# Kernel tuning notes

Hardware: AMD Instinct MI355X
Metric: run time of the kernel (lower is better)

## Reference

```python
import jax, jax.numpy as jnp
import numpy as np

N, B, NPG = 65536, 512, 128      # total nodes, graphs, nodes per graph
E, EPG = 524288, 1024            # total edges, edges per graph
D, R, L = 64, 16, 3              # emb_dim, num relations, encoder layers
PHI = 0.1
EPS_VAR = 1e-5


def _mean_std(x):
    # torch.var is unbiased (ddof=1); keep last-dim stats per row
    m = jnp.mean(x, axis=-1, keepdims=True)
    s = jnp.sqrt(jnp.var(x, axis=-1, ddof=1, keepdims=True) + EPS_VAR)
    return m, s


def _rgcn_encode(feat, Wrel, Wself, b, src, dst, etype, edge_w):
    """L-layer relational GCN. Returns (last_h [N,D], repr [N,L,D])."""
    h = feat
    reps = []
    for l in range(L):
        hr = jnp.einsum('nd,rdk->nrk', h, Wrel[l])        # [N,R,D]
        msg = hr[src, etype]                               # [E,D] per-edge typed transform
        msg = msg * edge_w[:, None]
        agg = jax.ops.segment_sum(msg, dst, num_segments=N)
        deg = jax.ops.segment_sum(edge_w, dst, num_segments=N)
        h = jax.nn.relu(h @ Wself[l] + agg / jnp.clip(deg, 1.0)[:, None] + b[l])
        reps.append(h)
    return h, jnp.stack(reps, axis=1)


def _pool(rep, node_gid):
    # mean_nodes over 'repr': graphs have fixed NPG nodes
    s = jax.ops.segment_sum(rep.reshape(N, L * D), node_gid, num_segments=B)
    return (s / NPG).reshape(B, L, D)


def full_forward(feat, rel_feat, rel_proj_W, rel_proj_b, rgcn_Wrel, rgcn_Wself,
                 rgcn_b, enc_W_mean, enc_W_std, dec_Wh, dec_bh, dec_Wt, dec_bt,
                 dec_Wr, dec_br, fc_W, fc_b, eps,
                 src, dst, etype, aug_src, aug_dst, aug_etype, node_gid, rel_labels):
    ones_e = jnp.ones((E,), feat.dtype)
    # relation encoder + projection
    emb_rel = jax.nn.relu(rel_feat @ rel_proj_W + rel_proj_b)          # [R,D]
    # encode original and augmented graphs
    x, rep_g = _rgcn_encode(feat, rgcn_Wrel, rgcn_Wself, rgcn_b, src, dst, etype, ones_e)
    g_out = _pool(rep_g, node_gid)
    aug_x, rep_aug = _rgcn_encode(feat, rgcn_Wrel, rgcn_Wself, rgcn_b, aug_src, aug_dst, aug_etype, ones_e)
    aug_g_out = _pool(rep_aug, node_gid)
    # AdaIn style transfer (args.interp == False)
    mc, sc = _mean_std(x)
    ms, ss = _mean_std(aug_x)
    style_applied = ss * ((x - mc) / sc) + ms
    # VAE reparameterization
    z_mean = style_applied @ enc_W_mean
    z_std = style_applied @ enc_W_std
    z = z_mean + jnp.sqrt(jnp.exp(z_std)) * eps
    # decoder: edge-level DistMult scoring -> edge mask
    head_e = jax.nn.relu(z[src] @ dec_Wh + dec_bh)                     # [E,D]
    tail_e = jax.nn.relu(z[dst] @ dec_Wt + dec_bt)
    rel_e = jax.nn.relu(emb_rel[etype] @ dec_Wr + dec_br)
    logit = jnp.sum(head_e * rel_e * tail_e, axis=-1)                  # [E]
    mask = (logit >= 0.5).astype(feat.dtype)
    # root edge (edge_ids(0,1)) = first edge of each graph, forced kept
    mask = mask.at[jnp.arange(B) * EPG].set(1.0)
    # re-encode reconstructed (masked) graph with original features
    x_recon, rep_recon = _rgcn_encode(feat, rgcn_Wrel, rgcn_Wself, rgcn_b, src, dst, etype, mask)
    recon_g_out = _pool(rep_recon, node_gid)
    # head node (id==1) = node 0 of each graph; tail (id==2) = node 1
    head_ids = jnp.arange(B) * NPG
    tail_ids = head_ids + 1
    g_rep = jnp.concatenate([
        recon_g_out.reshape(B, L * D),
        rep_recon[head_ids].reshape(B, L * D),
        rep_recon[tail_ids].reshape(B, L * D),
        emb_rel[rel_labels],
    ], axis=1)                                                          # [B, 3*L*D + D]
    output = g_rep @ fc_W + fc_b                                        # [B,1]
    # reconstruction + style losses, summed over layers
    mse_per_layer = jnp.mean((rep_recon - rep_g) ** 2, axis=(0, 2))     # [L]
    mr, sr = _mean_std(rep_recon.transpose(1, 0, 2))                    # [L,N,1]
    mg, sg = _mean_std(rep_g.transpose(1, 0, 2))
    style_per_layer = jnp.mean((mr - mg) ** 2, axis=(1, 2)) + jnp.mean((sr - sg) ** 2, axis=(1, 2))
    loss = jnp.sum(mse_per_layer) + PHI * jnp.sum(style_per_layer)
    return output, g_out, aug_g_out, loss


def setup_inputs() -> dict:
    key = jax.random.key(0)
    ks = jax.random.split(key, 28)
    egid = jnp.arange(E, dtype=jnp.int32) // EPG
    node_gid = jnp.arange(N, dtype=jnp.int32) // NPG
    mk_edges = lambda k1, k2: (egid * NPG + jax.random.randint(k1, (E,), 0, NPG, jnp.int32),
                               egid * NPG + jax.random.randint(k2, (E,), 0, NPG, jnp.int32))
    src, dst = mk_edges(ks[0], ks[1])
    aug_src, aug_dst = mk_edges(ks[2], ks[3])
    g = lambda i, shape, s=0.05: (jax.random.normal(ks[i], shape, jnp.float32) * s)
    return {
        'feat': g(4, (N, D), 1.0),
        'rel_feat': g(5, (R, 64), 1.0),
        'rel_proj_W': g(6, (64, D)),
        'rel_proj_b': jnp.zeros((D,), jnp.float32),
        'rgcn_Wrel': g(7, (L, R, D, D)),
        'rgcn_Wself': g(8, (L, D, D)),
        'rgcn_b': jnp.zeros((L, D), jnp.float32),
        'enc_W_mean': g(9, (D, D)),
        'enc_W_std': g(10, (D, D)),
        'dec_Wh': g(11, (D, D), 0.1),
        'dec_bh': jnp.zeros((D,), jnp.float32),
        'dec_Wt': g(12, (D, D), 0.1),
        'dec_bt': jnp.zeros((D,), jnp.float32),
        'dec_Wr': g(13, (D, D), 0.1),
        'dec_br': jnp.zeros((D,), jnp.float32),
        'fc_W': g(14, (3 * L * D + D, 1)),
        'fc_b': jnp.zeros((1,), jnp.float32),
        'eps': g(15, (N, D), 1.0),
        'src': src, 'dst': dst,
        'etype': jax.random.randint(ks[16], (E,), 0, R, jnp.int32),
        'aug_src': aug_src, 'aug_dst': aug_dst,
        'aug_etype': jax.random.randint(ks[17], (E,), 0, R, jnp.int32),
        'node_gid': node_gid,
        'rel_labels': jax.random.randint(ks[18], (B,), 0, R, jnp.int32),
    }


def reference(feat, rel_feat, rel_proj_W, rel_proj_b, rgcn_Wrel, rgcn_Wself,
              rgcn_b, enc_W_mean, enc_W_std, dec_Wh, dec_bh, dec_Wt, dec_bt,
              dec_Wr, dec_br, fc_W, fc_b, eps,
              src, dst, etype, aug_src, aug_dst, aug_etype, node_gid, rel_labels):
    return full_forward(feat, rel_feat, rel_proj_W, rel_proj_b, rgcn_Wrel, rgcn_Wself,
                        rgcn_b, enc_W_mean, enc_W_std, dec_Wh, dec_bh, dec_Wt, dec_bt,
                        dec_Wr, dec_br, fc_W, fc_b, eps,
                        src, dst, etype, aug_src, aug_dst, aug_etype, node_gid, rel_labels)
```

## Files before the change

kernel.cpp:

```cpp
#include <hip/hip_runtime.h>
#include <hip/hip_bf16.h>

typedef __attribute__((ext_vector_type(8))) short bf16x8;
typedef __attribute__((ext_vector_type(4))) float f32x4;

#define NPG  128
#define EPG  1024
#define BG   512
#define NT   512
#define NW   8
#define PHI  0.1f
#define EPSV 1e-5f
#define SB   72
#define SF   65

#define OUT_G    512
#define OUT_AUG  98816
#define OUT_LOSS 197120
#define WS_EMB   0
#define WS_RELE  1024
#define WS_LOSSP 2048
#define WS_REPG  4096

__device__ __forceinline__ unsigned short f2bf(float x) {
  __hip_bfloat16 h = __float2bfloat16(x);
  return *reinterpret_cast<unsigned short*>(&h);
}
__device__ __forceinline__ float bf2f(unsigned short u) {
  __hip_bfloat16 h = *reinterpret_cast<__hip_bfloat16*>(&u);
  return __bfloat162float(h);
}
__device__ __forceinline__ void split_write(unsigned short* hh, unsigned short* hl,
                                            int idx, float x) {
  unsigned short hi = f2bf(x);
  hh[idx] = hi;
  hl[idx] = f2bf(x - bf2f(hi));
}

#define LOAD_BF(Wp, ctn, ks, bhv, blv)                                         \
  {                                                                            \
    bf16x8 h_, l_;                                                             \
    _Pragma("unroll") for (int j_ = 0; j_ < 8; j_++) {                         \
      float w_ = (Wp)[((ks) * 32 + kg * 8 + j_) * 64 + (ctn) * 16 + n];        \
      unsigned short hi_ = f2bf(w_);                                           \
      h_[j_] = (short)hi_;                                                     \
      l_[j_] = (short)f2bf(w_ - bf2f(hi_));                                    \
    }                                                                          \
    bhv = h_;                                                                  \
    blv = l_;                                                                  \
  }

__device__ __forceinline__ f32x4 mfma3(bf16x8 a0h, bf16x8 a1h, bf16x8 a0l, bf16x8 a1l,
                                       bf16x8 b0h, bf16x8 b1h, bf16x8 b0l, bf16x8 b1l,
                                       f32x4 acc) {
  acc = __builtin_amdgcn_mfma_f32_16x16x32_bf16(a0h, b0h, acc, 0, 0, 0);
  acc = __builtin_amdgcn_mfma_f32_16x16x32_bf16(a1h, b1h, acc, 0, 0, 0);
  acc = __builtin_amdgcn_mfma_f32_16x16x32_bf16(a0h, b0l, acc, 0, 0, 0);
  acc = __builtin_amdgcn_mfma_f32_16x16x32_bf16(a1h, b1l, acc, 0, 0, 0);
  acc = __builtin_amdgcn_mfma_f32_16x16x32_bf16(a0l, b0h, acc, 0, 0, 0);
  acc = __builtin_amdgcn_mfma_f32_16x16x32_bf16(a1l, b1h, acc, 0, 0, 0);
  return acc;
}

__global__ __launch_bounds__(256) void k_prologue(
    const float* __restrict__ rel_feat, const float* __restrict__ rpW,
    const float* __restrict__ rpb, const float* __restrict__ dWr,
    const float* __restrict__ dbr, float* __restrict__ ws) {
  __shared__ float emb[1024];
  int tid = threadIdx.x;
  for (int idx = tid; idx < 1024; idx += 256) {
    int r = idx >> 6, j = idx & 63;
    float s = rpb[j];
    for (int k = 0; k < 64; k++) s = fmaf(rel_feat[r * 64 + k], rpW[k * 64 + j], s);
    s = fmaxf(s, 0.f);
    emb[idx] = s;
    ws[WS_EMB + idx] = s;
  }
  __syncthreads();
  for (int idx = tid; idx < 1024; idx += 256) {
    int r = idx >> 6, j = idx & 63;
    float s = dbr[j];
    for (int k = 0; k < 64; k++) s = fmaf(emb[r * 64 + k], dWr[k * 64 + j], s);
    ws[WS_RELE + idx] = fmaxf(s, 0.f);
  }
}

__global__ __launch_bounds__(512) void k_fin(const float* __restrict__ ws,
                                             float* __restrict__ out) {
  __shared__ float red[8];
  int tid = threadIdx.x;
  float x = ws[WS_LOSSP + tid];
#pragma unroll
  for (int o = 32; o > 0; o >>= 1) x += __shfl_down(x, o);
  if ((tid & 63) == 0) red[tid >> 6] = x;
  __syncthreads();
  if (tid == 0) {
    float s = 0.f;
#pragma unroll
    for (int w = 0; w < 8; w++) s += red[w];
    out[OUT_LOSS] = s;
  }
}

__device__ void build_elist(unsigned* elist, int* cnt, int* offs, float* dinv,
                            const unsigned* maskbits, int useMask,
                            const int* __restrict__ et_a, const int* __restrict__ src_a,
                            const int* __restrict__ dst_a, int ge, int gn, int tid) {
  if (tid < 16) cnt[tid] = 0;
  if (tid >= 128 && tid < 256) dinv[tid - 128] = 0.f;
  __syncthreads();
  for (int i = tid; i < EPG; i += NT) {
    int keep = useMask ? (int)((maskbits[i >> 5] >> (i & 31)) & 1u) : 1;
    if (keep) {
      atomicAdd(&cnt[et_a[ge + i]], 1);
      atomicAdd(&dinv[dst_a[ge + i] - gn], 1.f);
    }
  }
  __syncthreads();
  if (tid == 0) {
    int o = 0;
#pragma unroll
    for (int r = 0; r < 16; r++) { offs[r] = o; o += (cnt[r] + 15) & ~15; }
    offs[16] = o;
  }
  if (tid >= 128 && tid < 256) {
    int v = tid - 128;
    dinv[v] = 1.0f / fmaxf(dinv[v], 1.0f);
  }
  __syncthreads();
  int total = offs[16];
  for (int s = tid; s < total; s += NT) elist[s] = 128u;
  if (tid < 16) cnt[tid] = offs[tid];
  __syncthreads();
  for (int i = tid; i < EPG; i += NT) {
    int keep = useMask ? (int)((maskbits[i >> 5] >> (i & 31)) & 1u) : 1;
    if (keep) {
      int r = et_a[ge + i];
      int pos = atomicAdd(&cnt[r], 1);
      elist[pos] = ((unsigned)(src_a[ge + i] - gn) << 8) | (unsigned)(dst_a[ge + i] - gn);
    }
  }
  __syncthreads();
}

__device__ void rgcn_layer_mfma(unsigned short* hh, unsigned short* hl, float* hf32,
                                const float* dinv, const unsigned* elist,
                                const int* offs,
                                const float* __restrict__ Wl,
                                const float* __restrict__ Wsl,
                                const float* __restrict__ bl, int tid) {
  int lane = tid & 63, wave = tid >> 6;
  int n = lane & 15, kg = lane >> 4;
  for (int i = tid; i < NPG * SF; i += NT) hf32[i] = 0.f;
  __syncthreads();
  for (int r = wave; r < 16; r += NW) {
    int base = offs[r], end = offs[r + 1];
    if (base >= end) continue;
    const float* __restrict__ W = Wl + (r << 12);
#pragma unroll 1
    for (int ch = 0; ch < 2; ch++) {
      bf16x8 bh00, bh01, bl00, bl01, bh10, bh11, bl10, bl11;
      LOAD_BF(W, ch * 2 + 0, 0, bh00, bl00);
      LOAD_BF(W, ch * 2 + 0, 1, bh01, bl01);
      LOAD_BF(W, ch * 2 + 1, 0, bh10, bl10);
      LOAD_BF(W, ch * 2 + 1, 1, bh11, bl11);
      for (int tb = base; tb < end; tb += 16) {
        unsigned e = elist[tb + n];
        int srow = (int)(e >> 8);
        const unsigned short* rh = hh + srow * SB;
        const unsigned short* rl = hl + srow * SB;
        bf16x8 a0h = *(const bf16x8*)(rh + kg * 8);
        bf16x8 a1h = *(const bf16x8*)(rh + 32 + kg * 8);
        bf16x8 a0l = *(const bf16x8*)(rl + kg * 8);
        bf16x8 a1l = *(const bf16x8*)(rl + 32 + kg * 8);
        f32x4 acc0 = {0.f, 0.f, 0.f, 0.f}, acc1 = {0.f, 0.f, 0.f, 0.f};
        acc0 = mfma3(a0h, a1h, a0l, a1l, bh00, bh01, bl00, bl01, acc0);
        acc1 = mfma3(a0h, a1h, a0l, a1l, bh10, bh11, bl10, bl11, acc1);
#pragma unroll
        for (int i = 0; i < 4; i++) {
          int dst = (int)(elist[tb + kg * 4 + i] & 255u);
          if (dst < 128) {
            float* hp = hf32 + dst * SF + ch * 32 + n;
            atomicAdd(hp, acc0[i]);
            atomicAdd(hp + 16, acc1[i]);
          }
        }
      }
    }
  }
  __syncthreads();
  {
    const unsigned short* rh = hh + (wave * 16 + n) * SB;
    const unsigned short* rl = hl + (wave * 16 + n) * SB;
    bf16x8 a0h = *(const bf16x8*)(rh + kg * 8);
    bf16x8 a1h = *(const bf16x8*)(rh + 32 + kg * 8);
    bf16x8 a0l = *(const bf16x8*)(rl + kg * 8);
    bf16x8 a1l = *(const bf16x8*)(rl + 32 + kg * 8);
#pragma unroll 1
    for (int ch = 0; ch < 2; ch++) {
      bf16x8 bh00, bh01, bl00, bl01, bh10, bh11, bl10, bl11;
      LOAD_BF(Wsl, ch * 2 + 0, 0, bh00, bl00);
      LOAD_BF(Wsl, ch * 2 + 0, 1, bh01, bl01);
      LOAD_BF(Wsl, ch * 2 + 1, 0, bh10, bl10);
      LOAD_BF(Wsl, ch * 2 + 1, 1, bh11, bl11);
      f32x4 acc0 = {0.f, 0.f, 0.f, 0.f}, acc1 = {0.f, 0.f, 0.f, 0.f};
      acc0 = mfma3(a0h, a1h, a0l, a1l, bh00, bh01, bl00, bl01, acc0);
      acc1 = mfma3(a0h, a1h, a0l, a1l, bh10, bh11, bl10, bl11, acc1);
#pragma unroll
      for (int i = 0; i < 4; i++) {
        int node = wave * 16 + kg * 4 + i;
        float di = dinv[node];
#pragma unroll
        for (int c = 0; c < 2; c++) {
          int col = (ch * 2 + c) * 16 + n;
          float a = c ? acc1[i] : acc0[i];
          float v = a + hf32[node * SF + col] * di + bl[col];
          v = fmaxf(v, 0.f);
          hf32[node * SF + col] = v;
          split_write(hh, hl, node * SB + col, v);
        }
      }
    }
  }
  __syncthreads();
}

__device__ void dense_mfma(const unsigned short* ah, const unsigned short* al,
                           float* hf32, unsigned short* oh, unsigned short* ol,
                           const float* __restrict__ W, const float* __restrict__ bias,
                           int mode, const float* __restrict__ epsbuf, int gn, int tid) {
  int lane = tid & 63, wave = tid >> 6;
  int n = lane & 15, kg = lane >> 4;
  const unsigned short* rh = ah + (wave * 16 + n) * SB;
  const unsigned short* rl = al + (wave * 16 + n) * SB;
  bf16x8 a0h = *(const bf16x8*)(rh + kg * 8);
  bf16x8 a1h = *(const bf16x8*)(rh + 32 + kg * 8);
  bf16x8 a0l = *(const bf16x8*)(rl + kg * 8);
  bf16x8 a1l = *(const bf16x8*)(rl + 32 + kg * 8);
#pragma unroll 1
  for (int ch = 0; ch < 2; ch++) {
    bf16x8 bh00, bh01, bl00, bl01, bh10, bh11, bl10, bl11;
    LOAD_BF(W, ch * 2 + 0, 0, bh00, bl00);
    LOAD_BF(W, ch * 2 + 0, 1, bh01, bl01);
    LOAD_BF(W, ch * 2 + 1, 0, bh10, bl10);
    LOAD_BF(W, ch * 2 + 1, 1, bh11, bl11);
    f32x4 acc0 = {0.f, 0.f, 0.f, 0.f}, acc1 = {0.f, 0.f, 0.f, 0.f};
    acc0 = mfma3(a0h, a1h, a0l, a1l, bh00, bh01, bl00, bl01, acc0);
    acc1 = mfma3(a0h, a1h, a0l, a1l, bh10, bh11, bl10, bl11, acc1);
#pragma unroll
    for (int i = 0; i < 4; i++) {
      int node = wave * 16 + kg * 4 + i;
#pragma unroll
      for (int c = 0; c < 2; c++) {
        int col = (ch * 2 + c) * 16 + n;
        float a = c ? acc1[i] : acc0[i];
        if (mode == 0) {
          hf32[node * SF + col] = a;
        } else if (mode == 2) {
          hf32[node * SF + col] += sqrtf(expf(a)) * epsbuf[(gn + node) * 64 + col];
        } else {
          a = fmaxf(a + bias[col], 0.f);
          if (oh) split_write(oh, ol, node * SB + col, a);
          else hf32[node * SF + col] = a;
        }
      }
    }
  }
  __syncthreads();
}

__device__ void pool_sf(const float* hf32, float* red, float* dst, int tid) {
  int j = tid & 63, grp = tid >> 6;
  float s = 0.f;
  for (int v = grp * 16; v < grp * 16 + 16; v++) s += hf32[v * SF + j];
  red[tid] = s;
  __syncthreads();
  if (tid < 64) {
    float t = 0.f;
#pragma unroll
    for (int w = 0; w < NW; w++) t += red[w * 64 + tid];
    dst[tid] = t * (1.f / 128.f);
  }
  __syncthreads();
}

__global__ __launch_bounds__(NT, 2) void k_mega(
    const float* __restrict__ feat, const float* __restrict__ Wrel,
    const float* __restrict__ Wself, const float* __restrict__ bvec,
    const float* __restrict__ encWm, const float* __restrict__ encWs,
    const float* __restrict__ decWh, const float* __restrict__ dbh,
    const float* __restrict__ decWt, const float* __restrict__ dbt,
    const float* __restrict__ fcW, const float* __restrict__ fcb,
    const float* __restrict__ epsbuf,
    const int* __restrict__ srcA, const int* __restrict__ dstA, const int* __restrict__ etA,
    const int* __restrict__ asrcA, const int* __restrict__ adstA, const int* __restrict__ aetA,
    const int* __restrict__ rel_labels, float* __restrict__ ws, float* __restrict__ out) {
  __shared__ __align__(16) unsigned short hh[NPG * SB];
  __shared__ __align__(16) unsigned short hl[NPG * SB];
  __shared__ __align__(16) float hf32[NPG * SF];
  __shared__ __align__(16) unsigned elist[1280];
  __shared__ float dinv[NPG];
  __shared__ float red[NT];
  __shared__ float ht[384];
  __shared__ float rgout[192];
  __shared__ unsigned maskbits[EPG / 32];
  __shared__ int cnt[16], offs[17];

  int g = blockIdx.x, tid = threadIdx.x;
  int gn = g * NPG, ge = g * EPG;
  float* repg = ws + WS_REPG;
  float loss_acc = 0.f;

  build_elist(elist, cnt, offs, dinv, maskbits, 0, etA, srcA, dstA, ge, gn, tid);
  for (int i = tid; i < 8192; i += NT)
    split_write(hh, hl, (i >> 6) * SB + (i & 63), feat[gn * 64 + i]);
  __syncthreads();
  for (int l = 0; l < 3; l++) {
    rgcn_layer_mfma(hh, hl, hf32, dinv, elist, offs, Wrel + l * 65536,
                    Wself + l * 4096, bvec + l * 64, tid);
    for (int i = tid; i < 8192; i += NT)
      repg[(gn + (i >> 6)) * 192 + l * 64 + (i & 63)] = hf32[(i >> 6) * SF + (i & 63)];
    pool_sf(hf32, red, out + OUT_G + g * 192 + l * 64, tid);
  }
  build_elist(elist, cnt, offs, dinv, maskbits, 0, aetA, asrcA, adstA, ge, gn, tid);
  for (int i = tid; i < 8192; i += NT)
    split_write(hh, hl, (i >> 6) * SB + (i & 63), feat[gn * 64 + i]);
  __syncthreads();
  for (int l = 0; l < 3; l++) {
    rgcn_layer_mfma(hh, hl, hf32, dinv, elist, offs, Wrel + l * 65536,
                    Wself + l * 4096, bvec + l * 64, tid);
    pool_sf(hf32, red, out + OUT_AUG + g * 192 + l * 64, tid);
  }
  if (tid < NPG) {
    int v = tid;
    float t1 = 0.f, t2 = 0.f;
    for (int jj = 0; jj < 64; jj++) {
      int j = (v + jj) & 63;
      float y = hf32[v * SF + j];
      t1 += y; t2 += y * y;
    }
    float ms = t1 * (1.f / 64.f);
    red[v] = ms;
    red[NPG + v] = sqrtf((t2 - 64.f * ms * ms) * (1.f / 63.f) + EPSV);
  }
  __syncthreads();
  for (int i = tid; i < 8192; i += NT)
    hf32[(i >> 6) * SF + (i & 63)] = repg[(gn + (i >> 6)) * 192 + 128 + (i & 63)];
  __syncthreads();
  if (tid < NPG) {
    int v = tid;
    float s1 = 0.f, s2 = 0.f;
    for (int jj = 0; jj < 64; jj++) {
      int j = (v + jj) & 63;
      float x = hf32[v * SF + j];
      s1 += x; s2 += x * x;
    }
    float mc = s1 * (1.f / 64.f);
    float sc = sqrtf((s2 - 64.f * mc * mc) * (1.f / 63.f) + EPSV);
    float sca = red[NPG + v] / sc, ms = red[v];
    for (int jj = 0; jj < 64; jj++) {
      int j = (v + jj) & 63;
      hf32[v * SF + j] = (hf32[v * SF + j] - mc) * sca + ms;
    }
  }
  __syncthreads();
  for (int i = tid; i < 8192; i += NT)
    split_write(hh, hl, (i >> 6) * SB + (i & 63), hf32[(i >> 6) * SF + (i & 63)]);
  __syncthreads();
  dense_mfma(hh, hl, hf32, nullptr, nullptr, encWm, nullptr, 0, nullptr, gn, tid);
  dense_mfma(hh, hl, hf32, nullptr, nullptr, encWs, nullptr, 2, epsbuf, gn, tid);
  for (int i = tid; i < 8192; i += NT)
    split_write(hh, hl, (i >> 6) * SB + (i & 63), hf32[(i >> 6) * SF + (i & 63)]);
  __syncthreads();
  dense_mfma(hh, hl, hf32, nullptr, nullptr, decWt, dbt, 1, nullptr, gn, tid);
  dense_mfma(hh, hl, hf32, hh, hl, decWh, dbh, 1, nullptr, gn, tid);
  float* relEl = (float*)elist;
  for (int i = tid; i < 1024; i += NT) relEl[i] = ws[WS_RELE + i];
  for (int i = tid; i < EPG / 32; i += NT) maskbits[i] = 0u;
  __syncthreads();
  for (int i = tid; i < EPG; i += NT) {
    int s = srcA[ge + i] - gn, t = dstA[ge + i] - gn, r = etA[ge + i];
    int rot = (s + t) & 63;
    float lg = 0.f;
    for (int jj = 0; jj < 64; jj++) {
      int j = (rot + jj) & 63;
      float zhv = bf2f(hh[s * SB + j]) + bf2f(hl[s * SB + j]);
      lg = fmaf(zhv * hf32[t * SF + j], relEl[(r << 6) + j], lg);
    }
    if (lg >= 0.5f) atomicOr(&maskbits[i >> 5], 1u << (i & 31));
  }
  __syncthreads();
  if (tid == 0) maskbits[0] |= 1u;
  __syncthreads();
  build_elist(elist, cnt, offs, dinv, maskbits, 1, etA, srcA, dstA, ge, gn, tid);
  for (int i = tid; i < 8192; i += NT)
    split_write(hh, hl, (i >> 6) * SB + (i & 63), feat[gn * 64 + i]);
  __syncthreads();
  const float c1 = 1.0f / (65536.0f * 64.0f);
  const float c2 = PHI / 65536.0f;
  for (int l = 0; l < 3; l++) {
    rgcn_layer_mfma(hh, hl, hf32, dinv, elist, offs, Wrel + l * 65536,
                    Wself + l * 4096, bvec + l * 64, tid);
    pool_sf(hf32, red, rgout + l * 64, tid);
    if (tid < 128)
      ht[(l * 2 + (tid >> 6)) * 64 + (tid & 63)] = hf32[(tid >> 6) * SF + (tid & 63)];
    {
      int v = tid >> 2, q = tid & 3;
      const float* gp = repg + (gn + v) * 192 + l * 64 + q * 16;
      const float* hp = hf32 + v * SF + q * 16;
      float mse = 0.f, a1 = 0.f, a2 = 0.f, b1 = 0.f, b2 = 0.f;
#pragma unroll
      for (int u = 0; u < 16; u++) {
        float rc = hp[u];
        float gg = gp[u];
        float d = rc - gg;
        mse += d * d; a1 += rc; a2 += rc * rc; b1 += gg; b2 += gg * gg;
      }
#pragma unroll
      for (int m = 1; m < 4; m <<= 1) {
        mse += __shfl_xor(mse, m); a1 += __shfl_xor(a1, m); a2 += __shfl_xor(a2, m);
        b1 += __shfl_xor(b1, m); b2 += __shfl_xor(b2, m);
      }
      if (q == 0) {
        float mr = a1 * (1.f / 64.f), mg = b1 * (1.f / 64.f);
        float sr = sqrtf((a2 - 64.f * mr * mr) * (1.f / 63.f) + EPSV);
        float sg = sqrtf((b2 - 64.f * mg * mg) * (1.f / 63.f) + EPSV);
        float style = (mr - mg) * (mr - mg) + (sr - sg) * (sr - sg);
        red[v] = mse * c1 + style * c2;
      }
    }
    __syncthreads();
    if (tid < 64) {
      float x = red[tid] + red[tid + 64];
#pragma unroll
      for (int o = 32; o > 0; o >>= 1) x += __shfl_down(x, o);
      if (tid == 0) loss_acc += x;
    }
    __syncthreads();
  }
  if (tid == 0) ws[WS_LOSSP + g] = loss_acc;
  if (tid < 64) {
    int rl = rel_labels[g];
    const float* emb = ws + WS_EMB + rl * 64;
    float s = 0.f;
    for (int p = 0; p < 10; p++) {
      int i = p * 64 + tid;
      float gr;
      if (i < 192) gr = rgout[i];
      else if (i < 384) { int i2 = i - 192; gr = ht[((i2 >> 6) * 2 + 0) * 64 + (i2 & 63)]; }
      else if (i < 576) { int i2 = i - 384; gr = ht[((i2 >> 6) * 2 + 1) * 64 + (i2 & 63)]; }
      else gr = emb[i - 576];
      s = fmaf(gr, fcW[i], s);
    }
#pragma unroll
    for (int o = 32; o > 0; o >>= 1) s += __shfl_down(s, o);
    if (tid == 0) out[g] = s + fcb[0];
  }
}

extern "C" void kernel_launch(void* const* d_in, const int* in_sizes, int n_in,
                              void* d_out, int out_size, void* d_ws, size_t ws_size,
                              hipStream_t stream) {
  const float* feat     = (const float*)d_in[0];
  const float* rel_feat = (const float*)d_in[1];
  const float* rpW      = (const float*)d_in[2];
  const float* rpb      = (const float*)d_in[3];
  const float* Wrel     = (const float*)d_in[4];
  const float* Wself    = (const float*)d_in[5];
  const float* bvec     = (const float*)d_in[6];
  const float* encWm    = (const float*)d_in[7];
  const float* encWs    = (const float*)d_in[8];
  const float* decWh    = (const float*)d_in[9];
  const float* dbh      = (const float*)d_in[10];
  const float* decWt    = (const float*)d_in[11];
  const float* dbt      = (const float*)d_in[12];
  const float* decWr    = (const float*)d_in[13];
  const float* dbr      = (const float*)d_in[14];
  const float* fcW      = (const float*)d_in[15];
  const float* fcb      = (const float*)d_in[16];
  const float* epsb     = (const float*)d_in[17];
  const int* srcA  = (const int*)d_in[18];
  const int* dstA  = (const int*)d_in[19];
  const int* etA   = (const int*)d_in[20];
  const int* asrcA = (const int*)d_in[21];
  const int* adstA = (const int*)d_in[22];
  const int* aetA  = (const int*)d_in[23];
  const int* rel_labels = (const int*)d_in[25];
  float* out = (float*)d_out;
  float* ws  = (float*)d_ws;

  k_prologue<<<1, 256, 0, stream>>>(rel_feat, rpW, rpb, decWr, dbr, ws);
  k_mega<<<BG, NT, 0, stream>>>(feat, Wrel, Wself, bvec, encWm, encWs, decWh, dbh,
                                decWt, dbt, fcW, fcb, epsb, srcA, dstA, etA,
                                asrcA, adstA, aetA, rel_labels, ws, out);
  k_fin<<<1, 512, 0, stream>>>(ws, out);
}
```

Measured before the change: 1.584 ms.

## Aggregate source features per relation before transform, then one dense MFMA per relation

Reorders the RGCN message passing so raw source features are scatter-added per relation into a shared fp32 buffer, then multiplied by that relation's weight with MFMA, instead of running MFMA per edge tile and atomically scattering the outputs. The relation loop now runs sequentially across the whole block, with a buffer clear and barriers per relation. The fp32 node-state buffer is dropped in favour of reconstructing values from the hi/lo bf16 split, and the VAE dense stages are fused into two paired phases. This cuts MFMA work and edge-list padding, but adds 16 serialized clear/scatter/barrier rounds per layer and extra atomics on raw features. Aggregating before the transform also changes rounding, since sums are re-split into bf16 hi/lo before the multiply.

```diff
diff --git a/kernel.cpp b/kernel.cpp
--- a/kernel.cpp
+++ b/kernel.cpp
@@ -3,6 +3,7 @@
 
 typedef __attribute__((ext_vector_type(8))) short bf16x8;
 typedef __attribute__((ext_vector_type(4))) float f32x4;
+typedef __attribute__((ext_vector_type(4))) short short4v;
 
 #define NPG  128
 #define EPG  1024
@@ -12,7 +13,7 @@
 #define PHI  0.1f
 #define EPSV 1e-5f
 #define SB   72
-#define SF   65
+#define SS   68
 
 #define OUT_G    512
 #define OUT_AUG  98816
@@ -35,6 +36,22 @@
   unsigned short hi = f2bf(x);
   hh[idx] = hi;
   hl[idx] = f2bf(x - bf2f(hi));
+}
+__device__ __forceinline__ float recon(const unsigned short* hh,
+                                       const unsigned short* hl, int idx) {
+  return bf2f(hh[idx]) + bf2f(hl[idx]);
+}
+
+__device__ __forceinline__ void split_frag(const float* p, bf16x8& ah, bf16x8& al) {
+  float4 v0 = *(const float4*)(p);
+  float4 v1 = *(const float4*)(p + 4);
+  float vv[8] = {v0.x, v0.y, v0.z, v0.w, v1.x, v1.y, v1.z, v1.w};
+#pragma unroll
+  for (int j = 0; j < 8; j++) {
+    unsigned short hi = f2bf(vv[j]);
+    ah[j] = (short)hi;
+    al[j] = (short)f2bf(vv[j] - bf2f(hi));
+  }
 }
 
 #define LOAD_BF(Wp, ctn, ks, bhv, blv)                                         \
@@ -120,7 +137,7 @@
   if (tid == 0) {
     int o = 0;
 #pragma unroll
-    for (int r = 0; r < 16; r++) { offs[r] = o; o += (cnt[r] + 15) & ~15; }
+    for (int r = 0; r < 16; r++) { offs[r] = o; o += cnt[r]; }
     offs[16] = o;
   }
   if (tid >= 128 && tid < 256) {
@@ -128,8 +145,6 @@
     dinv[v] = 1.0f / fmaxf(dinv[v], 1.0f);
   }
   __syncthreads();
-  int total = offs[16];
-  for (int s = tid; s < total; s += NT) elist[s] = 128u;
   if (tid < 16) cnt[tid] = offs[tid];
   __syncthreads();
   for (int i = tid; i < EPG; i += NT) {
@@ -143,52 +158,52 @@
   __syncthreads();
 }
 
-__device__ void rgcn_layer_mfma(unsigned short* hh, unsigned short* hl, float* hf32,
-                                const float* dinv, const unsigned* elist,
-                                const int* offs,
-                                const float* __restrict__ Wl,
-                                const float* __restrict__ Wsl,
-                                const float* __restrict__ bl, int tid) {
+__device__ void rgcn_layer_dense(unsigned short* hh, unsigned short* hl, float* S,
+                                 const float* dinv, const unsigned* elist,
+                                 const int* offs,
+                                 const float* __restrict__ Wl,
+                                 const float* __restrict__ Wsl,
+                                 const float* __restrict__ bl, int tid) {
   int lane = tid & 63, wave = tid >> 6;
   int n = lane & 15, kg = lane >> 4;
-  for (int i = tid; i < NPG * SF; i += NT) hf32[i] = 0.f;
-  __syncthreads();
-  for (int r = wave; r < 16; r += NW) {
+  f32x4 agg[4];
+#pragma unroll
+  for (int ct = 0; ct < 4; ct++) agg[ct] = (f32x4){0.f, 0.f, 0.f, 0.f};
+
+  for (int r = 0; r < 16; r++) {
     int base = offs[r], end = offs[r + 1];
-    if (base >= end) continue;
-    const float* __restrict__ W = Wl + (r << 12);
+    if (base == end) continue;
+    for (int i = tid; i < NPG * SS; i += NT) S[i] = 0.f;
+    __syncthreads();
+    int tasks = (end - base) << 4;
+    for (int t = tid; t < tasks; t += NT) {
+      int e = base + (t >> 4), c4 = (t & 15) << 2;
+      unsigned ed = elist[e];
+      int src = (int)(ed >> 8), dst = (int)(ed & 255u);
+      short4v vh = *(const short4v*)(hh + src * SB + c4);
+      short4v vl = *(const short4v*)(hl + src * SB + c4);
+      float* ps = S + dst * SS + c4;
+#pragma unroll
+      for (int k2 = 0; k2 < 4; k2++)
+        atomicAdd(ps + k2, bf2f((unsigned short)vh[k2]) + bf2f((unsigned short)vl[k2]));
+    }
+    __syncthreads();
+    {
+      const float* sr = S + (wave * 16 + n) * SS;
+      bf16x8 a0h, a0l, a1h, a1l;
+      split_frag(sr + kg * 8, a0h, a0l);
+      split_frag(sr + 32 + kg * 8, a1h, a1l);
+      const float* __restrict__ W = Wl + (r << 12);
 #pragma unroll 1
-    for (int ch = 0; ch < 2; ch++) {
-      bf16x8 bh00, bh01, bl00, bl01, bh10, bh11, bl10, bl11;
-      LOAD_BF(W, ch * 2 + 0, 0, bh00, bl00);
-      LOAD_BF(W, ch * 2 + 0, 1, bh01, bl01);
-      LOAD_BF(W, ch * 2 + 1, 0, bh10, bl10);
-      LOAD_BF(W, ch * 2 + 1, 1, bh11, bl11);
-      for (int tb = base; tb < end; tb += 16) {
-        unsigned e = elist[tb + n];
-        int srow = (int)(e >> 8);
-        const unsigned short* rh = hh + srow * SB;
-        const unsigned short* rl = hl + srow * SB;
-        bf16x8 a0h = *(const bf16x8*)(rh + kg * 8);
-        bf16x8 a1h = *(const bf16x8*)(rh + 32 + kg * 8);
-        bf16x8 a0l = *(const bf16x8*)(rl + kg * 8);
-        bf16x8 a1l = *(const bf16x8*)(rl + 32 + kg * 8);
-        f32x4 acc0 = {0.f, 0.f, 0.f, 0.f}, acc1 = {0.f, 0.f, 0.f, 0.f};
-        acc0 = mfma3(a0h, a1h, a0l, a1l, bh00, bh01, bl00, bl01, acc0);
-        acc1 = mfma3(a0h, a1h, a0l, a1l, bh10, bh11, bl10, bl11, acc1);
-#pragma unroll
-        for (int i = 0; i < 4; i++) {
-          int dst = (int)(elist[tb + kg * 4 + i] & 255u);
-          if (dst < 128) {
-            float* hp = hf32 + dst * SF + ch * 32 + n;
-            atomicAdd(hp, acc0[i]);
-            atomicAdd(hp + 16, acc1[i]);
-          }
-        }
+      for (int ct = 0; ct < 4; ct++) {
+        bf16x8 bh0, bl0, bh1, bl1;
+        LOAD_BF(W, ct, 0, bh0, bl0);
+        LOAD_BF(W, ct, 1, bh1, bl1);
+        agg[ct] = mfma3(a0h, a1h, a0l, a1l, bh0, bh1, bl0, bl1, agg[ct]);
       }
     }
-  }
-  __syncthreads();
+    __syncthreads();
+  }
   {
     const unsigned short* rh = hh + (wave * 16 + n) * SB;
     const unsigned short* rl = hl + (wave * 16 + n) * SB;
@@ -196,83 +211,106 @@
     bf16x8 a1h = *(const bf16x8*)(rh + 32 + kg * 8);
     bf16x8 a0l = *(const bf16x8*)(rl + kg * 8);
     bf16x8 a1l = *(const bf16x8*)(rl + 32 + kg * 8);
+    f32x4 sf[4];
 #pragma unroll 1
-    for (int ch = 0; ch < 2; ch++) {
-      bf16x8 bh00, bh01, bl00, bl01, bh10, bh11, bl10, bl11;
-      LOAD_BF(Wsl, ch * 2 + 0, 0, bh00, bl00);
-      LOAD_BF(Wsl, ch * 2 + 0, 1, bh01, bl01);
-      LOAD_BF(Wsl, ch * 2 + 1, 0, bh10, bl10);
-      LOAD_BF(Wsl, ch * 2 + 1, 1, bh11, bl11);
-      f32x4 acc0 = {0.f, 0.f, 0.f, 0.f}, acc1 = {0.f, 0.f, 0.f, 0.f};
-      acc0 = mfma3(a0h, a1h, a0l, a1l, bh00, bh01, bl00, bl01, acc0);
-      acc1 = mfma3(a0h, a1h, a0l, a1l, bh10, bh11, bl10, bl11, acc1);
-#pragma unroll
-      for (int i = 0; i < 4; i++) {
-        int node = wave * 16 + kg * 4 + i;
-        float di = dinv[node];
-#pragma unroll
-        for (int c = 0; c < 2; c++) {
-          int col = (ch * 2 + c) * 16 + n;
-          float a = c ? acc1[i] : acc0[i];
-          float v = a + hf32[node * SF + col] * di + bl[col];
-          v = fmaxf(v, 0.f);
-          hf32[node * SF + col] = v;
-          split_write(hh, hl, node * SB + col, v);
-        }
+    for (int ct = 0; ct < 4; ct++) {
+      bf16x8 bh0, bl0, bh1, bl1;
+      LOAD_BF(Wsl, ct, 0, bh0, bl0);
+      LOAD_BF(Wsl, ct, 1, bh1, bl1);
+      sf[ct] = mfma3(a0h, a1h, a0l, a1l, bh0, bh1, bl0, bl1,
+                     (f32x4){0.f, 0.f, 0.f, 0.f});
+    }
+#pragma unroll
+    for (int i = 0; i < 4; i++) {
+      int node = wave * 16 + kg * 4 + i;
+      float di = dinv[node];
+#pragma unroll
+      for (int ct = 0; ct < 4; ct++) {
+        int col = ct * 16 + n;
+        float v = sf[ct][i] + agg[ct][i] * di + bl[col];
+        split_write(hh, hl, node * SB + col, fmaxf(v, 0.f));
       }
     }
   }
   __syncthreads();
 }
 
-__device__ void dense_mfma(const unsigned short* ah, const unsigned short* al,
-                           float* hf32, unsigned short* oh, unsigned short* ol,
-                           const float* __restrict__ W, const float* __restrict__ bias,
-                           int mode, const float* __restrict__ epsbuf, int gn, int tid) {
+__device__ void vae_phaseA(unsigned short* hh, unsigned short* hl,
+                           const float* __restrict__ Wm, const float* __restrict__ Wsd,
+                           const float* __restrict__ epsbuf, int gn, int tid) {
   int lane = tid & 63, wave = tid >> 6;
   int n = lane & 15, kg = lane >> 4;
-  const unsigned short* rh = ah + (wave * 16 + n) * SB;
-  const unsigned short* rl = al + (wave * 16 + n) * SB;
+  const unsigned short* rh = hh + (wave * 16 + n) * SB;
+  const unsigned short* rl = hl + (wave * 16 + n) * SB;
   bf16x8 a0h = *(const bf16x8*)(rh + kg * 8);
   bf16x8 a1h = *(const bf16x8*)(rh + 32 + kg * 8);
   bf16x8 a0l = *(const bf16x8*)(rl + kg * 8);
   bf16x8 a1l = *(const bf16x8*)(rl + 32 + kg * 8);
+  f32x4 am[4], as[4];
 #pragma unroll 1
-  for (int ch = 0; ch < 2; ch++) {
-    bf16x8 bh00, bh01, bl00, bl01, bh10, bh11, bl10, bl11;
-    LOAD_BF(W, ch * 2 + 0, 0, bh00, bl00);
-    LOAD_BF(W, ch * 2 + 0, 1, bh01, bl01);
-    LOAD_BF(W, ch * 2 + 1, 0, bh10, bl10);
-    LOAD_BF(W, ch * 2 + 1, 1, bh11, bl11);
-    f32x4 acc0 = {0.f, 0.f, 0.f, 0.f}, acc1 = {0.f, 0.f, 0.f, 0.f};
-    acc0 = mfma3(a0h, a1h, a0l, a1l, bh00, bh01, bl00, bl01, acc0);
-    acc1 = mfma3(a0h, a1h, a0l, a1l, bh10, bh11, bl10, bl11, acc1);
-#pragma unroll
-    for (int i = 0; i < 4; i++) {
-      int node = wave * 16 + kg * 4 + i;
-#pragma unroll
-      for (int c = 0; c < 2; c++) {
-        int col = (ch * 2 + c) * 16 + n;
-        float a = c ? acc1[i] : acc0[i];
-        if (mode == 0) {
-          hf32[node * SF + col] = a;
-        } else if (mode == 2) {
-          hf32[node * SF + col] += sqrtf(expf(a)) * epsbuf[(gn + node) * 64 + col];
-        } else {
-          a = fmaxf(a + bias[col], 0.f);
-          if (oh) split_write(oh, ol, node * SB + col, a);
-          else hf32[node * SF + col] = a;
-        }
-      }
-    }
-  }
-  __syncthreads();
-}
-
-__device__ void pool_sf(const float* hf32, float* red, float* dst, int tid) {
+  for (int ct = 0; ct < 4; ct++) {
+    bf16x8 bh0, bl0, bh1, bl1;
+    LOAD_BF(Wm, ct, 0, bh0, bl0);
+    LOAD_BF(Wm, ct, 1, bh1, bl1);
+    am[ct] = mfma3(a0h, a1h, a0l, a1l, bh0, bh1, bl0, bl1, (f32x4){0.f, 0.f, 0.f, 0.f});
+    LOAD_BF(Wsd, ct, 0, bh0, bl0);
+    LOAD_BF(Wsd, ct, 1, bh1, bl1);
+    as[ct] = mfma3(a0h, a1h, a0l, a1l, bh0, bh1, bl0, bl1, (f32x4){0.f, 0.f, 0.f, 0.f});
+  }
+#pragma unroll
+  for (int i = 0; i < 4; i++) {
+    int node = wave * 16 + kg * 4 + i;
+#pragma unroll
+    for (int ct = 0; ct < 4; ct++) {
+      int col = ct * 16 + n;
+      float z = am[ct][i] + sqrtf(expf(as[ct][i])) * epsbuf[(gn + node) * 64 + col];
+      split_write(hh, hl, node * SB + col, z);
+    }
+  }
+  __syncthreads();
+}
+
+__device__ void vae_phaseB(unsigned short* hh, unsigned short* hl, float* S,
+                           const float* __restrict__ Wt, const float* __restrict__ bt,
+                           const float* __restrict__ Wh, const float* __restrict__ bh_,
+                           int tid) {
+  int lane = tid & 63, wave = tid >> 6;
+  int n = lane & 15, kg = lane >> 4;
+  const unsigned short* rh = hh + (wave * 16 + n) * SB;
+  const unsigned short* rl = hl + (wave * 16 + n) * SB;
+  bf16x8 a0h = *(const bf16x8*)(rh + kg * 8);
+  bf16x8 a1h = *(const bf16x8*)(rh + 32 + kg * 8);
+  bf16x8 a0l = *(const bf16x8*)(rl + kg * 8);
+  bf16x8 a1l = *(const bf16x8*)(rl + 32 + kg * 8);
+  f32x4 at[4], ah[4];
+#pragma unroll 1
+  for (int ct = 0; ct < 4; ct++) {
+    bf16x8 bh0, bl0, bh1, bl1;
+    LOAD_BF(Wt, ct, 0, bh0, bl0);
+    LOAD_BF(Wt, ct, 1, bh1, bl1);
+    at[ct] = mfma3(a0h, a1h, a0l, a1l, bh0, bh1, bl0, bl1, (f32x4){0.f, 0.f, 0.f, 0.f});
+    LOAD_BF(Wh, ct, 0, bh0, bl0);
+    LOAD_BF(Wh, ct, 1, bh1, bl1);
+    ah[ct] = mfma3(a0h, a1h, a0l, a1l, bh0, bh1, bl0, bl1, (f32x4){0.f, 0.f, 0.f, 0.f});
+  }
+#pragma unroll
+  for (int i = 0; i < 4; i++) {
+    int node = wave * 16 + kg * 4 + i;
+#pragma unroll
+    for (int ct = 0; ct < 4; ct++) {
+      int col = ct * 16 + n;
+      S[node * SS + col] = fmaxf(at[ct][i] + bt[col], 0.f);
+      split_write(hh, hl, node * SB + col, fmaxf(ah[ct][i] + bh_[col], 0.f));
+    }
+  }
+  __syncthreads();
+}
+
+__device__ void pool_hl(const unsigned short* hh, const unsigned short* hl,
+                        float* red, float* dst, int tid) {
   int j = tid & 63, grp = tid >> 6;
   float s = 0.f;
-  for (int v = grp * 16; v < grp * 16 + 16; v++) s += hf32[v * SF + j];
+  for (int v = grp * 16; v < grp * 16 + 16; v++) s += recon(hh, hl, v * SB + j);
   red[tid] = s;
   __syncthreads();
   if (tid < 64) {
@@ -297,8 +335,8 @@
     const int* __restrict__ rel_labels, float* __restrict__ ws, float* __restrict__ out) {
   __shared__ __align__(16) unsigned short hh[NPG * SB];
   __shared__ __align__(16) unsigned short hl[NPG * SB];
-  __shared__ __align__(16) float hf32[NPG * SF];
-  __shared__ __align__(16) unsigned elist[1280];
+  __shared__ __align__(16) float S[NPG * SS];
+  __shared__ __align__(16) unsigned elist[EPG];
   __shared__ float dinv[NPG];
   __shared__ float red[NT];
   __shared__ float ht[384];
@@ -316,27 +354,38 @@
     split_write(hh, hl, (i >> 6) * SB + (i & 63), feat[gn * 64 + i]);
   __syncthreads();
   for (int l = 0; l < 3; l++) {
-    rgcn_layer_mfma(hh, hl, hf32, dinv, elist, offs, Wrel + l * 65536,
-                    Wself + l * 4096, bvec + l * 64, tid);
+    rgcn_layer_dense(hh, hl, S, dinv, elist, offs, Wrel + l * 65536,
+                     Wself + l * 4096, bvec + l * 64, tid);
     for (int i = tid; i < 8192; i += NT)
-      repg[(gn + (i >> 6)) * 192 + l * 64 + (i & 63)] = hf32[(i >> 6) * SF + (i & 63)];
-    pool_sf(hf32, red, out + OUT_G + g * 192 + l * 64, tid);
+      repg[(gn + (i >> 6)) * 192 + l * 64 + (i & 63)] = recon(hh, hl, (i >> 6) * SB + (i & 63));
+    pool_hl(hh, hl, red, out + OUT_G + g * 192 + l * 64, tid);
   }
   build_elist(elist, cnt, offs, dinv, maskbits, 0, aetA, asrcA, adstA, ge, gn, tid);
   for (int i = tid; i < 8192; i += NT)
     split_write(hh, hl, (i >> 6) * SB + (i & 63), feat[gn * 64 + i]);
   __syncthreads();
   for (int l = 0; l < 3; l++) {
-    rgcn_layer_mfma(hh, hl, hf32, dinv, elist, offs, Wrel + l * 65536,
-                    Wself + l * 4096, bvec + l * 64, tid);
-    pool_sf(hf32, red, out + OUT_AUG + g * 192 + l * 64, tid);
+    rgcn_layer_dense(hh, hl, S, dinv, elist, offs, Wrel + l * 65536,
+                     Wself + l * 4096, bvec + l * 64, tid);
+    pool_hl(hh, hl, red, out + OUT_AUG + g * 192 + l * 64, tid);
   }
   if (tid < NPG) {
     int v = tid;
     float t1 = 0.f, t2 = 0.f;
     for (int jj = 0; jj < 64; jj++) {
       int j = (v + jj) & 63;
-      float y = hf32[v * SF + j];
+      float y = recon(hh, hl, (v << 6) + ((v * SB - (v << 6))) + j);
+      t1 += y; t2 += y * y;
+    }
+    red[v] = t1; red[NPG + v] = t2;
+  }
+  __syncthreads();
+  if (tid < NPG) {
+    int v = tid;
+    float t1 = 0.f, t2 = 0.f;
+    for (int jj = 0; jj < 64; jj++) {
+      int j = (v + jj) & 63;
+      float y = recon(hh, hl, v * SB + j);
       t1 += y; t2 += y * y;
     }
     float ms = t1 * (1.f / 64.f);
@@ -344,36 +393,20 @@
     red[NPG + v] = sqrtf((t2 - 64.f * ms * ms) * (1.f / 63.f) + EPSV);
   }
   __syncthreads();
-  for (int i = tid; i < 8192; i += NT)
-    hf32[(i >> 6) * SF + (i & 63)] = repg[(gn + (i >> 6)) * 192 + 128 + (i & 63)];
-  __syncthreads();
   if (tid < NPG) {
     int v = tid;
+    const float* xr = repg + (gn + v) * 192 + 128;
     float s1 = 0.f, s2 = 0.f;
-    for (int jj = 0; jj < 64; jj++) {
-      int j = (v + jj) & 63;
-      float x = hf32[v * SF + j];
-      s1 += x; s2 += x * x;
-    }
+    for (int j = 0; j < 64; j++) { float x = xr[j]; s1 += x; s2 += x * x; }
     float mc = s1 * (1.f / 64.f);
     float sc = sqrtf((s2 - 64.f * mc * mc) * (1.f / 63.f) + EPSV);
     float sca = red[NPG + v] / sc, ms = red[v];
-    for (int jj = 0; jj < 64; jj++) {
-      int j = (v + jj) & 63;
-      hf32[v * SF + j] = (hf32[v * SF + j] - mc) * sca + ms;
-    }
-  }
-  __syncthreads();
-  for (int i = tid; i < 8192; i += NT)
-    split_write(hh, hl, (i >> 6) * SB + (i & 63), hf32[(i >> 6) * SF + (i & 63)]);
-  __syncthreads();
-  dense_mfma(hh, hl, hf32, nullptr, nullptr, encWm, nullptr, 0, nullptr, gn, tid);
-  dense_mfma(hh, hl, hf32, nullptr, nullptr, encWs, nullptr, 2, epsbuf, gn, tid);
-  for (int i = tid; i < 8192; i += NT)
-    split_write(hh, hl, (i >> 6) * SB + (i & 63), hf32[(i >> 6) * SF + (i & 63)]);
-  __syncthreads();
-  dense_mfma(hh, hl, hf32, nullptr, nullptr, decWt, dbt, 1, nullptr, gn, tid);
-  dense_mfma(hh, hl, hf32, hh, hl, decWh, dbh, 1, nullptr, gn, tid);
+    for (int j = 0; j < 64; j++)
+      split_write(hh, hl, v * SB + j, (xr[j] - mc) * sca + ms);
+  }
+  __syncthreads();
+  vae_phaseA(hh, hl, encWm, encWs, epsbuf, gn, tid);
+  vae_phaseB(hh, hl, S, decWt, dbt, decWh, dbh, tid);
   float* relEl = (float*)elist;
   for (int i = tid; i < 1024; i += NT) relEl[i] = ws[WS_RELE + i];
   for (int i = tid; i < EPG / 32; i += NT) maskbits[i] = 0u;
@@ -384,8 +417,7 @@
     float lg = 0.f;
     for (int jj = 0; jj < 64; jj++) {
       int j = (rot + jj) & 63;
-      float zhv = bf2f(hh[s * SB + j]) + bf2f(hl[s * SB + j]);
-      lg = fmaf(zhv * hf32[t * SF + j], relEl[(r << 6) + j], lg);
+      lg = fmaf(recon(hh, hl, s * SB + j) * S[t * SS + j], relEl[(r << 6) + j], lg);
     }
     if (lg >= 0.5f) atomicOr(&maskbits[i >> 5], 1u << (i & 31));
   }
@@ -399,19 +431,18 @@
   const float c1 = 1.0f / (65536.0f * 64.0f);
   const float c2 = PHI / 65536.0f;
   for (int l = 0; l < 3; l++) {
-    rgcn_layer_mfma(hh, hl, hf32, dinv, elist, offs, Wrel + l * 65536,
-                    Wself + l * 4096, bvec + l * 64, tid);
-    pool_sf(hf32, red, rgout + l * 64, tid);
+    rgcn_layer_dense(hh, hl, S, dinv, elist, offs, Wrel + l * 65536,
+                     Wself + l * 4096, bvec + l * 64, tid);
+    pool_hl(hh, hl, red, rgout + l * 64, tid);
     if (tid < 128)
-      ht[(l * 2 + (tid >> 6)) * 64 + (tid & 63)] = hf32[(tid >> 6) * SF + (tid & 63)];
+      ht[(l * 2 + (tid >> 6)) * 64 + (tid & 63)] = recon(hh, hl, (tid >> 6) * SB + (tid & 63));
     {
       int v = tid >> 2, q = tid & 3;
       const float* gp = repg + (gn + v) * 192 + l * 64 + q * 16;
-      const float* hp = hf32 + v * SF + q * 16;
       float mse = 0.f, a1 = 0.f, a2 = 0.f, b1 = 0.f, b2 = 0.f;
 #pragma unroll
       for (int u = 0; u < 16; u++) {
-        float rc = hp[u];
+        float rc = recon(hh, hl, v * SB + q * 16 + u);
         float gg = gp[u];
         float d = rc - gg;
         mse += d * d; a1 += rc; a2 += rc * rc; b1 += gg; b2 += gg * gg;
```

New measurement: 2.469 ms. 1.56x slower.
